# Kernel tuning notes

Measured on AMD Instinct MI355X. Metric: run time of the kernel, lower is better.

The kernel has to match this reference:

```python
import jax, jax.numpy as jnp
import numpy as np

B, NQ, C, H, W, HEADS = 8, 300, 256, 64, 64, 8
HD = C // HEADS
SCALING = float(HD) ** (-0.5)


def setup_inputs() -> dict:
    key = jax.random.key(0)
    ks = jax.random.split(key, 12)
    pts = jax.random.uniform(ks[3], (B, NQ, 2), jnp.float32)
    pts = pts * jnp.array([W - 1, H - 1], jnp.float32)  # (x, y) in pixel coords
    s = 1.0 / np.sqrt(C)
    return {
        "query": jax.random.normal(ks[0], (B, NQ, C), jnp.float32),
        "key": jax.random.normal(ks[1], (B, C, H, W), jnp.float32),
        "value": jax.random.normal(ks[2], (B, C, H, W), jnp.float32),
        "sampling_points": pts,
        "Wq": jax.random.normal(ks[4], (C, C), jnp.float32) * s,
        "bq": jnp.zeros((C,), jnp.float32),
        "Wk": jax.random.normal(ks[5], (C, C), jnp.float32) * s,
        "bk": jnp.zeros((C,), jnp.float32),
        "Wv": jax.random.normal(ks[6], (C, C), jnp.float32) * s,
        "bv": jnp.zeros((C,), jnp.float32),
        "Wo": jax.random.normal(ks[7], (C, C), jnp.float32) * s,
        "bo": jnp.zeros((C,), jnp.float32),
    }


def _sample_rows(feat, y):
    # feat: [b,heads,hd,h,w]; y: [b,q] float row coordinate.
    # Returns feat linearly interpolated in y for every column: [b,q,heads,hd,w]
    h = feat.shape[3]
    y0f = jnp.clip(jnp.floor(y), 0.0, h - 1)
    wy = y - y0f
    y0 = y0f.astype(jnp.int32)
    y1 = jnp.clip(y0 + 1, 0, h - 1)
    g = jax.vmap(lambda f, idx: f[:, :, idx, :])  # per-batch -> [heads,hd,q,w]
    r = g(feat, y0) * (1.0 - wy)[:, None, None, :, None] + g(feat, y1) * wy[:, None, None, :, None]
    return jnp.transpose(r, (0, 3, 1, 2, 4))


def _sample_cols(feat, x):
    # feat: [b,heads,hd,h,w]; x: [b,q] float col coordinate -> [b,q,heads,hd,h]
    w = feat.shape[4]
    x0f = jnp.clip(jnp.floor(x), 0.0, w - 1)
    wx = x - x0f
    x0 = x0f.astype(jnp.int32)
    x1 = jnp.clip(x0 + 1, 0, w - 1)
    g = jax.vmap(lambda f, idx: f[:, :, :, idx])  # per-batch -> [heads,hd,h,q]
    c = g(feat, x0) * (1.0 - wx)[:, None, None, None, :] + g(feat, x1) * wx[:, None, None, None, :]
    return jnp.transpose(c, (0, 4, 1, 2, 3))


def reference(query, key, value, sampling_points, Wq, bq, Wk, bk, Wv, bv, Wo, bo):
    b, nq, c = query.shape
    h, w = key.shape[2], key.shape[3]
    pq = (query @ Wq.T + bq) * SCALING                     # [b,nq,C]
    pk = jnp.einsum('oc,bchw->bohw', Wk, key) + bk[None, :, None, None]
    pv = jnp.einsum('oc,bchw->bohw', Wv, value) + bv[None, :, None, None]
    pq = pq.reshape(b, nq, HEADS, HD)
    pk = pk.reshape(b, HEADS, HD, h, w)
    pv = pv.reshape(b, HEADS, HD, h, w)
    x, y = sampling_points[..., 0], sampling_points[..., 1]
    # criss-cross weights: row through y (w samples) + column through x (h samples)
    k_row = _sample_rows(pk, y)                            # [b,q,heads,hd,w]
    k_col = _sample_cols(pk, x)                            # [b,q,heads,hd,h]
    w_row = jnp.einsum('bqnd,bqndw->bqnw', pq, k_row)
    w_col = jnp.einsum('bqnd,bqndk->bqnk', pq, k_col)
    attn = jax.nn.softmax(jnp.concatenate([w_row, w_col], axis=-1), axis=-1)
    a_row, a_col = attn[..., :w], attn[..., w:]
    v_row = _sample_rows(pv, y)
    v_col = _sample_cols(pv, x)
    out = jnp.einsum('bqnw,bqndw->bqnd', a_row, v_row) + jnp.einsum('bqnk,bqndk->bqnd', a_col, v_col)
    out = out.reshape(b, nq, c)
    return out @ Wo.T + bo
```

## Files before the change

kernel.cpp:

```cpp
#include <hip/hip_runtime.h>
#include <hip/hip_bf16.h>
#include <math.h>

constexpr int cB = 8, cNQ = 300, cC = 256, cH = 64, cW = 64, cHEADS = 8, cHD = 32;
constexpr int cHW = cH * cW;
constexpr int cM = cB * cNQ;
constexpr float cSCALE = 0.1767766952966369f;

typedef __bf16 bf16_t;
typedef bf16_t bf16x4 __attribute__((ext_vector_type(4)));
typedef bf16_t bf16x8 __attribute__((ext_vector_type(8)));
typedef float f32x4 __attribute__((ext_vector_type(4)));
typedef _Float16 f16_t;
typedef f16_t f16x2 __attribute__((ext_vector_type(2)));
typedef f16_t f16x8 __attribute__((ext_vector_type(8)));

__device__ __forceinline__ float dot2acc(f16x2 a, f16x2 b, float c) {
#if __has_builtin(__builtin_amdgcn_fdot2)
  return __builtin_amdgcn_fdot2(a, b, c, false);
#else
  return c + (float)a.x * (float)b.x + (float)a.y * (float)b.y;
#endif
}

__global__ __launch_bounds__(256) void proj_mfma_k(
    const float* __restrict__ X, const float* __restrict__ Wt,
    const float* __restrict__ bias, float* __restrict__ out,
    f16_t* __restrict__ out_h, float scale, int M) {
  __shared__ bf16_t Xs[128 * 64];
  __shared__ bf16_t Ws[64 * 64];
  int m0 = blockIdx.x * 128;
  int o0 = blockIdx.y * 64;
  int tid = threadIdx.x;
  int lane = tid & 63, w = tid >> 6;
  int moff = (w & 1) * 64, ooff = (w >> 1) * 32;
  int l15 = lane & 15, l4 = lane >> 4;
  int srow = tid >> 1;
  int schalf = (tid & 1) * 32;
  int wo_l = tid >> 2;
  int wcg = (tid & 3) * 16;

  f32x4 acc[4][2];
#pragma unroll
  for (int m = 0; m < 4; ++m)
#pragma unroll
    for (int n = 0; n < 2; ++n) acc[m][n] = (f32x4){0.f, 0.f, 0.f, 0.f};

  for (int c0 = 0; c0 < cC; c0 += 64) {
    {
      int mrow = min(m0 + srow, M - 1);
      const float4* xr = (const float4*)(X + (size_t)mrow * cC + c0 + schalf);
      int sw = (srow & 7) * 8;
#pragma unroll
      for (int i = 0; i < 4; ++i) {
        float4 a = xr[i * 2], b4 = xr[i * 2 + 1];
        bf16x8 v = {(bf16_t)a.x, (bf16_t)a.y, (bf16_t)a.z, (bf16_t)a.w,
                    (bf16_t)b4.x, (bf16_t)b4.y, (bf16_t)b4.z, (bf16_t)b4.w};
        *(bf16x8*)&Xs[srow * 64 + ((schalf + i * 8) ^ sw)] = v;
      }
    }
    {
      const float4* wr = (const float4*)(Wt + (size_t)(o0 + wo_l) * cC + c0 + wcg);
      float4 a = wr[0], b4 = wr[1], c4 = wr[2], d4 = wr[3];
      bf16x8 w0 = {(bf16_t)a.x, (bf16_t)a.y, (bf16_t)a.z, (bf16_t)a.w,
                   (bf16_t)b4.x, (bf16_t)b4.y, (bf16_t)b4.z, (bf16_t)b4.w};
      bf16x8 w1 = {(bf16_t)c4.x, (bf16_t)c4.y, (bf16_t)c4.z, (bf16_t)c4.w,
                   (bf16_t)d4.x, (bf16_t)d4.y, (bf16_t)d4.z, (bf16_t)d4.w};
      int sw = (wo_l & 7) * 8;
      *(bf16x8*)&Ws[wo_l * 64 + (wcg ^ sw)] = w0;
      *(bf16x8*)&Ws[wo_l * 64 + ((wcg + 8) ^ sw)] = w1;
    }
    __syncthreads();
#pragma unroll
    for (int s = 0; s < 2; ++s) {
      int c8 = s * 32 + l4 * 8;
      bf16x8 afr[4], bfr[2];
#pragma unroll
      for (int m = 0; m < 4; ++m) {
        int r = moff + m * 16 + l15;
        afr[m] = *(const bf16x8*)&Xs[r * 64 + (c8 ^ ((r & 7) * 8))];
      }
#pragma unroll
      for (int n = 0; n < 2; ++n) {
        int r = ooff + n * 16 + l15;
        bfr[n] = *(const bf16x8*)&Ws[r * 64 + (c8 ^ ((r & 7) * 8))];
      }
#pragma unroll
      for (int m = 0; m < 4; ++m)
#pragma unroll
        for (int n = 0; n < 2; ++n)
          acc[m][n] = __builtin_amdgcn_mfma_f32_16x16x32_bf16(
              afr[m], bfr[n], acc[m][n], 0, 0, 0);
    }
    __syncthreads();
  }

  float b0 = bias[o0 + ooff + l15];
  float b1 = bias[o0 + ooff + 16 + l15];
#pragma unroll
  for (int m = 0; m < 4; ++m) {
    int mr = m0 + moff + m * 16 + l4 * 4;
#pragma unroll
    for (int reg = 0; reg < 4; ++reg) {
      if (mr + reg < M) {
        float v0 = (acc[m][0][reg] + b0) * scale;
        float v1 = (acc[m][1][reg] + b1) * scale;
        if (out_h) {
          out_h[(size_t)(mr + reg) * cC + o0 + ooff + l15] = (f16_t)v0;
          out_h[(size_t)(mr + reg) * cC + o0 + ooff + 16 + l15] = (f16_t)v1;
        } else {
          out[(size_t)(mr + reg) * cC + o0 + ooff + l15] = v0;
          out[(size_t)(mr + reg) * cC + o0 + ooff + 16 + l15] = v1;
        }
      }
    }
  }
}

__global__ __launch_bounds__(512) void proj_kv_mfma_k(
    const float* __restrict__ key, const float* __restrict__ value,
    const float* __restrict__ Wk, const float* __restrict__ bk,
    const float* __restrict__ Wv, const float* __restrict__ bv,
    f16_t* __restrict__ pkT, f16_t* __restrict__ pvT) {
  int z = blockIdx.z;
  int b = z >> 1;
  bool isv = z & 1;
  const float* X = (isv ? value : key) + (size_t)b * cC * cHW;
  const float* Wm = isv ? Wv : Wk;
  const float* bb = isv ? bv : bk;
  f16_t* outT = (isv ? pvT : pkT) + (size_t)b * cHEADS * cHW * cHD;
  int hw0 = blockIdx.x * 128;
  int o0 = blockIdx.y * 128;

  __shared__ bf16_t Xs[2][128 * 64];
  __shared__ bf16_t Wf[2][16 * 64 * 8];

  int tid = threadIdx.x;
  int lane = tid & 63, w = tid >> 6;
  int l15 = lane & 15, l4 = lane >> 4;
  int cq = tid & 15;
  int hwg = tid >> 4;
  int wo_l = tid >> 2;
  int wcg = (tid & 3) * 16;
  int wks = wcg >> 5;
  int wl4 = (wcg & 31) >> 3;
  int wnt = wo_l >> 4, wl15 = wo_l & 15;
  int hwoff = (w >> 2) * 64;
  int nb = (w & 3) * 2;

  const float* xbase = X + hw0 + hwg * 4;
  const float* wbase = Wm + (size_t)(o0 + wo_l) * cC + wcg;

  f32x4 acc[4][2];
#pragma unroll
  for (int m = 0; m < 4; ++m)
#pragma unroll
    for (int n = 0; n < 2; ++n) acc[m][n] = (f32x4){0.f, 0.f, 0.f, 0.f};

  float4 xr4[4];
  float4 wr[4];
  auto issue = [&](int c0) {
#pragma unroll
    for (int i = 0; i < 4; ++i)
      xr4[i] = *(const float4*)(xbase + (size_t)(c0 + cq * 4 + i) * cHW);
    const float4* p = (const float4*)(wbase + c0);
    wr[0] = p[0]; wr[1] = p[1]; wr[2] = p[2]; wr[3] = p[3];
  };

  issue(0);
#pragma unroll
  for (int s = 0; s < 4; ++s) {
    const int buf = s & 1;
#pragma unroll
    for (int j = 0; j < 4; ++j) {
      int row = hwg * 4 + j;
      bf16x4 v = {(bf16_t)xr4[0][j], (bf16_t)xr4[1][j],
                  (bf16_t)xr4[2][j], (bf16_t)xr4[3][j]};
      *(bf16x4*)&Xs[buf][row * 64 + ((cq * 4) ^ ((row & 7) * 8))] = v;
    }
    {
      bf16x8 v0 = {(bf16_t)wr[0].x, (bf16_t)wr[0].y, (bf16_t)wr[0].z, (bf16_t)wr[0].w,
                   (bf16_t)wr[1].x, (bf16_t)wr[1].y, (bf16_t)wr[1].z, (bf16_t)wr[1].w};
      bf16x8 v1 = {(bf16_t)wr[2].x, (bf16_t)wr[2].y, (bf16_t)wr[2].z, (bf16_t)wr[2].w,
                   (bf16_t)wr[3].x, (bf16_t)wr[3].y, (bf16_t)wr[3].z, (bf16_t)wr[3].w};
      *(bf16x8*)&Wf[buf][(size_t)((wks * 8 + wnt) * 64 + wl4 * 16 + wl15) * 8] = v0;
      *(bf16x8*)&Wf[buf][(size_t)((wks * 8 + wnt) * 64 + (wl4 + 1) * 16 + wl15) * 8] = v1;
    }
    if (s < 3) issue((s + 1) * 64);
    __syncthreads();
#pragma unroll
    for (int ks = 0; ks < 2; ++ks) {
      int c8 = ks * 32 + l4 * 8;
      bf16x8 bf0 = *(const bf16x8*)&Wf[buf][(size_t)((ks * 8 + nb) * 64 + lane) * 8];
      bf16x8 bf1 = *(const bf16x8*)&Wf[buf][(size_t)((ks * 8 + nb + 1) * 64 + lane) * 8];
#pragma unroll
      for (int m = 0; m < 4; ++m) {
        int r = hwoff + m * 16 + l15;
        bf16x8 a = *(const bf16x8*)&Xs[buf][r * 64 + (c8 ^ ((r & 7) * 8))];
        acc[m][0] = __builtin_amdgcn_mfma_f32_16x16x32_bf16(a, bf0, acc[m][0], 0, 0, 0);
        acc[m][1] = __builtin_amdgcn_mfma_f32_16x16x32_bf16(a, bf1, acc[m][1], 0, 0, 0);
      }
    }
  }

  int osub = o0 + nb * 16;
  int head = osub >> 5;
  f16_t* obase = outT + (size_t)head * cHW * cHD;
  float bias0 = bb[osub + l15];
  float bias1 = bb[osub + 16 + l15];
#pragma unroll
  for (int m = 0; m < 4; ++m) {
    int hwr = hwoff + m * 16 + l4 * 4;
#pragma unroll
    for (int reg = 0; reg < 4; ++reg) {
      int hw = hw0 + hwr + reg;
      size_t rowoff = (size_t)hw * cHD;
      obase[rowoff + l15] = (f16_t)(acc[m][0][reg] + bias0);
      obase[rowoff + 16 + l15] = (f16_t)(acc[m][1][reg] + bias1);
    }
  }
}

__global__ __launch_bounds__(256) void attn_k(
    const f16_t* __restrict__ pqh, const f16_t* __restrict__ pkT,
    const f16_t* __restrict__ pvT, const float* __restrict__ pts,
    float* __restrict__ out) {
  int bid = blockIdx.x;
  int xcd = bid & 7;
  int t = bid >> 3;
  int phase = (t >= cNQ) ? 1 : 0;
  int q = t - phase * cNQ;
  int g = xcd + 8 * phase;
  int b = g >> 1;
  int pair = g & 1;
  int lane = threadIdx.x & 63;
  int wid = threadIdx.x >> 6;
  int n = pair * 4 + wid;

  float x = pts[((size_t)b * cNQ + q) * 2 + 0];
  float y = pts[((size_t)b * cNQ + q) * 2 + 1];
  float y0f = fminf(fmaxf(floorf(y), 0.f), (float)(cH - 1));
  float x0f = fminf(fmaxf(floorf(x), 0.f), (float)(cW - 1));
  float wy = y - y0f, wx = x - x0f;
  int y0 = (int)y0f, y1 = min(y0 + 1, cH - 1);
  int x0 = (int)x0f, x1 = min(x0 + 1, cW - 1);

  size_t hoff = (size_t)(b * cHEADS + n) * cHW * cHD;
  const f16_t* kTb = pkT + hoff;
  const f16_t* vTb = pvT + hoff;

  int g16 = lane >> 2, ch = lane & 3;

  f16x8 qv = *(const f16x8*)(pqh + ((size_t)b * cNQ + q) * cC + n * cHD + ch * 8);
  const f16x2* qp = (const f16x2*)&qv;

  float wrowA[4], wcolA[4];
#pragma unroll
  for (int k = 0; k < 4; ++k) {
    int p = g16 * 4 + k;
    f16x8 a0 = *(const f16x8*)(kTb + (size_t)(y0 * cW + p) * cHD + ch * 8);
    f16x8 a1 = *(const f16x8*)(kTb + (size_t)(y1 * cW + p) * cHD + ch * 8);
    f16x8 b0 = *(const f16x8*)(kTb + (size_t)(p * cW + x0) * cHD + ch * 8);
    f16x8 b1 = *(const f16x8*)(kTb + (size_t)(p * cW + x1) * cHD + ch * 8);
    const f16x2* a0p = (const f16x2*)&a0;
    const f16x2* a1p = (const f16x2*)&a1;
    const f16x2* b0p = (const f16x2*)&b0;
    const f16x2* b1p = (const f16x2*)&b1;
    float s0 = 0.f, s1 = 0.f, t0 = 0.f, t1 = 0.f;
#pragma unroll
    for (int j2 = 0; j2 < 4; ++j2) {
      f16x2 qq = qp[j2];
      s0 = dot2acc(a0p[j2], qq, s0);
      s1 = dot2acc(a1p[j2], qq, s1);
      t0 = dot2acc(b0p[j2], qq, t0);
      t1 = dot2acc(b1p[j2], qq, t1);
    }
    float wrow = s0 + wy * (s1 - s0);
    float wcol = t0 + wx * (t1 - t0);
    wrow += __shfl_xor(wrow, 1, 64);
    wrow += __shfl_xor(wrow, 2, 64);
    wcol += __shfl_xor(wcol, 1, 64);
    wcol += __shfl_xor(wcol, 2, 64);
    wrowA[k] = wrow;
    wcolA[k] = wcol;
  }

  float m = -1e30f;
#pragma unroll
  for (int k = 0; k < 4; ++k) m = fmaxf(m, fmaxf(wrowA[k], wcolA[k]));
#pragma unroll
  for (int sh = 4; sh <= 32; sh <<= 1) m = fmaxf(m, __shfl_xor(m, sh, 64));
  float er[4], ec[4];
  float ssl = 0.f;
#pragma unroll
  for (int k = 0; k < 4; ++k) {
    er[k] = __expf(wrowA[k] - m);
    ec[k] = __expf(wcolA[k] - m);
    ssl += er[k] + ec[k];
  }
  float ssum = ssl;
#pragma unroll
  for (int sh = 4; sh <= 32; sh <<= 1) ssum += __shfl_xor(ssum, sh, 64);

  float omwy = 1.f - wy, omwx = 1.f - wx;
  float acc[8];
#pragma unroll
  for (int j = 0; j < 8; ++j) acc[j] = 0.f;
#pragma unroll
  for (int k = 0; k < 4; ++k) {
    int p = g16 * 4 + k;
    f16x8 r0 = *(const f16x8*)(vTb + (size_t)(y0 * cW + p) * cHD + ch * 8);
    f16x8 r1 = *(const f16x8*)(vTb + (size_t)(y1 * cW + p) * cHD + ch * 8);
    f16x8 c0 = *(const f16x8*)(vTb + (size_t)(p * cW + x0) * cHD + ch * 8);
    f16x8 c1 = *(const f16x8*)(vTb + (size_t)(p * cW + x1) * cHD + ch * 8);
    float wr0 = er[k] * omwy, wr1 = er[k] * wy;
    float wc0 = ec[k] * omwx, wc1 = ec[k] * wx;
#pragma unroll
    for (int j = 0; j < 8; ++j) {
      acc[j] += wr0 * (float)r0[j] + wr1 * (float)r1[j] +
                wc0 * (float)c0[j] + wc1 * (float)c1[j];
    }
  }
#pragma unroll
  for (int sh = 4; sh <= 32; sh <<= 1)
#pragma unroll
    for (int j = 0; j < 8; ++j) acc[j] += __shfl_xor(acc[j], sh, 64);

  float inv = 1.f / ssum;
  if (lane < 4) {
    float* op = out + ((size_t)b * cNQ + q) * cC + n * cHD + ch * 8;
    float4 o0 = {acc[0] * inv, acc[1] * inv, acc[2] * inv, acc[3] * inv};
    float4 o1 = {acc[4] * inv, acc[5] * inv, acc[6] * inv, acc[7] * inv};
    *(float4*)op = o0;
    *(float4*)(op + 4) = o1;
  }
}

extern "C" void kernel_launch(void* const* d_in, const int* in_sizes, int n_in,
                              void* d_out, int out_size, void* d_ws, size_t ws_size,
                              hipStream_t stream) {
  const float* query = (const float*)d_in[0];
  const float* key   = (const float*)d_in[1];
  const float* value = (const float*)d_in[2];
  const float* pts   = (const float*)d_in[3];
  const float* Wq = (const float*)d_in[4];
  const float* bq = (const float*)d_in[5];
  const float* Wk = (const float*)d_in[6];
  const float* bk = (const float*)d_in[7];
  const float* Wv = (const float*)d_in[8];
  const float* bv = (const float*)d_in[9];
  const float* Wo = (const float*)d_in[10];
  const float* bo = (const float*)d_in[11];
  float* out = (float*)d_out;

  const size_t kvsz = (size_t)cB * cC * cHW;
  f16_t* pqh = (f16_t*)d_ws;
  f16_t* pkT = pqh + (size_t)cM * cC;
  f16_t* pvT = pkT + kvsz;
  float* ao = (float*)(pvT + kvsz);

  proj_mfma_k<<<dim3((cM + 127) / 128, cC / 64), 256, 0, stream>>>(
      query, Wq, bq, nullptr, pqh, cSCALE, cM);
  proj_kv_mfma_k<<<dim3(cHW / 128, cC / 128, cB * 2), 512, 0, stream>>>(
      key, value, Wk, bk, Wv, bv, pkT, pvT);
  attn_k<<<cB * cNQ * 2, 256, 0, stream>>>(pqh, pkT, pvT, pts, ao);
  proj_mfma_k<<<dim3((cM + 127) / 128, cC / 64), 256, 0, stream>>>(
      ao, Wo, bo, out, nullptr, 1.0f, cM);
}
```

Measured before the change: 92.68 us.

## Overlap second-half K/V projection with first-half attention in a merged kernel

Splits the K/V projection by batch. The first four batches are projected alone. A merged kernel then interleaves blocks that project the last four batches with blocks that run attention for the first four batches, and a final kernel does attention for the remaining batches. The aim is to overlap compute-heavy MFMA projection with the gather-heavy attention and to cut idle time between dependent launches. In exchange it adds an extra synchronisation per projection stage, and the merged blocks reserve the full 512-thread and shared-memory footprint even on attention blocks, which may reduce occupancy.

```diff
diff --git a/kernel.cpp b/kernel.cpp
--- a/kernel.cpp
+++ b/kernel.cpp
@@ -117,25 +117,22 @@
   }
 }
 
-__global__ __launch_bounds__(512) void proj_kv_mfma_k(
+__device__ __forceinline__ void proj_kv_body(
+    int xb, int yb, int zb, int tid,
     const float* __restrict__ key, const float* __restrict__ value,
     const float* __restrict__ Wk, const float* __restrict__ bk,
     const float* __restrict__ Wv, const float* __restrict__ bv,
-    f16_t* __restrict__ pkT, f16_t* __restrict__ pvT) {
-  int z = blockIdx.z;
-  int b = z >> 1;
-  bool isv = z & 1;
+    f16_t* __restrict__ pkT, f16_t* __restrict__ pvT,
+    bf16_t* __restrict__ XsB, bf16_t* __restrict__ WfB) {
+  int b = zb >> 1;
+  bool isv = zb & 1;
   const float* X = (isv ? value : key) + (size_t)b * cC * cHW;
   const float* Wm = isv ? Wv : Wk;
   const float* bb = isv ? bv : bk;
   f16_t* outT = (isv ? pvT : pkT) + (size_t)b * cHEADS * cHW * cHD;
-  int hw0 = blockIdx.x * 128;
-  int o0 = blockIdx.y * 128;
-
-  __shared__ bf16_t Xs[2][128 * 64];
-  __shared__ bf16_t Wf[2][16 * 64 * 8];
-
-  int tid = threadIdx.x;
+  int hw0 = xb * 128;
+  int o0 = yb * 128;
+
   int lane = tid & 63, w = tid >> 6;
   int l15 = lane & 15, l4 = lane >> 4;
   int cq = tid & 15;
@@ -170,37 +167,39 @@
   issue(0);
 #pragma unroll
   for (int s = 0; s < 4; ++s) {
-    const int buf = s & 1;
+    bf16_t* Xs = XsB + (s & 1) * (128 * 64);
+    bf16_t* Wf = WfB + (s & 1) * (16 * 64 * 8);
 #pragma unroll
     for (int j = 0; j < 4; ++j) {
       int row = hwg * 4 + j;
       bf16x4 v = {(bf16_t)xr4[0][j], (bf16_t)xr4[1][j],
                   (bf16_t)xr4[2][j], (bf16_t)xr4[3][j]};
-      *(bf16x4*)&Xs[buf][row * 64 + ((cq * 4) ^ ((row & 7) * 8))] = v;
+      *(bf16x4*)&Xs[row * 64 + ((cq * 4) ^ ((row & 7) * 8))] = v;
     }
     {
       bf16x8 v0 = {(bf16_t)wr[0].x, (bf16_t)wr[0].y, (bf16_t)wr[0].z, (bf16_t)wr[0].w,
                    (bf16_t)wr[1].x, (bf16_t)wr[1].y, (bf16_t)wr[1].z, (bf16_t)wr[1].w};
       bf16x8 v1 = {(bf16_t)wr[2].x, (bf16_t)wr[2].y, (bf16_t)wr[2].z, (bf16_t)wr[2].w,
                    (bf16_t)wr[3].x, (bf16_t)wr[3].y, (bf16_t)wr[3].z, (bf16_t)wr[3].w};
-      *(bf16x8*)&Wf[buf][(size_t)((wks * 8 + wnt) * 64 + wl4 * 16 + wl15) * 8] = v0;
-      *(bf16x8*)&Wf[buf][(size_t)((wks * 8 + wnt) * 64 + (wl4 + 1) * 16 + wl15) * 8] = v1;
+      *(bf16x8*)&Wf[(size_t)((wks * 8 + wnt) * 64 + wl4 * 16 + wl15) * 8] = v0;
+      *(bf16x8*)&Wf[(size_t)((wks * 8 + wnt) * 64 + (wl4 + 1) * 16 + wl15) * 8] = v1;
     }
     if (s < 3) issue((s + 1) * 64);
     __syncthreads();
 #pragma unroll
     for (int ks = 0; ks < 2; ++ks) {
       int c8 = ks * 32 + l4 * 8;
-      bf16x8 bf0 = *(const bf16x8*)&Wf[buf][(size_t)((ks * 8 + nb) * 64 + lane) * 8];
-      bf16x8 bf1 = *(const bf16x8*)&Wf[buf][(size_t)((ks * 8 + nb + 1) * 64 + lane) * 8];
+      bf16x8 bf0 = *(const bf16x8*)&Wf[(size_t)((ks * 8 + nb) * 64 + lane) * 8];
+      bf16x8 bf1 = *(const bf16x8*)&Wf[(size_t)((ks * 8 + nb + 1) * 64 + lane) * 8];
 #pragma unroll
       for (int m = 0; m < 4; ++m) {
         int r = hwoff + m * 16 + l15;
-        bf16x8 a = *(const bf16x8*)&Xs[buf][r * 64 + (c8 ^ ((r & 7) * 8))];
+        bf16x8 a = *(const bf16x8*)&Xs[r * 64 + (c8 ^ ((r & 7) * 8))];
         acc[m][0] = __builtin_amdgcn_mfma_f32_16x16x32_bf16(a, bf0, acc[m][0], 0, 0, 0);
         acc[m][1] = __builtin_amdgcn_mfma_f32_16x16x32_bf16(a, bf1, acc[m][1], 0, 0, 0);
       }
     }
+    if (s < 3) __syncthreads();
   }
 
   int osub = o0 + nb * 16;
@@ -221,20 +220,13 @@
   }
 }
 
-__global__ __launch_bounds__(256) void attn_k(
+__device__ __forceinline__ void attn_body(
+    int b, int pair, int q, int subtid,
     const f16_t* __restrict__ pqh, const f16_t* __restrict__ pkT,
     const f16_t* __restrict__ pvT, const float* __restrict__ pts,
     float* __restrict__ out) {
-  int bid = blockIdx.x;
-  int xcd = bid & 7;
-  int t = bid >> 3;
-  int phase = (t >= cNQ) ? 1 : 0;
-  int q = t - phase * cNQ;
-  int g = xcd + 8 * phase;
-  int b = g >> 1;
-  int pair = g & 1;
-  int lane = threadIdx.x & 63;
-  int wid = threadIdx.x >> 6;
+  int lane = subtid & 63;
+  int wid = subtid >> 6;
   int n = pair * 4 + wid;
 
   float x = pts[((size_t)b * cNQ + q) * 2 + 0];
@@ -334,6 +326,55 @@
     *(float4*)op = o0;
     *(float4*)(op + 4) = o1;
   }
+}
+
+__global__ __launch_bounds__(512) void proj_kv_half_k(
+    const float* __restrict__ key, const float* __restrict__ value,
+    const float* __restrict__ Wk, const float* __restrict__ bk,
+    const float* __restrict__ Wv, const float* __restrict__ bv,
+    f16_t* __restrict__ pkT, f16_t* __restrict__ pvT, int zbase) {
+  __shared__ bf16_t Xs[2][128 * 64];
+  __shared__ bf16_t Wf[2][16 * 64 * 8];
+  proj_kv_body(blockIdx.x, blockIdx.y, zbase + blockIdx.z, threadIdx.x,
+               key, value, Wk, bk, Wv, bv, pkT, pvT, &Xs[0][0], &Wf[0][0]);
+}
+
+__global__ __launch_bounds__(512) void merged_k(
+    const float* __restrict__ key, const float* __restrict__ value,
+    const float* __restrict__ Wk, const float* __restrict__ bk,
+    const float* __restrict__ Wv, const float* __restrict__ bv,
+    f16_t* __restrict__ pkT, f16_t* __restrict__ pvT,
+    const f16_t* __restrict__ pqh, const float* __restrict__ pts,
+    float* __restrict__ ao) {
+  __shared__ bf16_t Xs[2][128 * 64];
+  __shared__ bf16_t Wf[2][16 * 64 * 8];
+  int bid = blockIdx.x;
+  int g = bid >> 3, sub8 = bid & 7;
+  int npg = (g * 32) / 107;
+  bool is_proj = ((g + 1) * 32) / 107 > npg;
+  if (is_proj) {
+    int p = npg * 8 + sub8;
+    proj_kv_body(p & 31, (p >> 5) & 1, 8 + (p >> 6), threadIdx.x,
+                 key, value, Wk, bk, Wv, bv, pkT, pvT, &Xs[0][0], &Wf[0][0]);
+  } else {
+    int ag = g - npg;
+    int b = sub8 >> 1;
+    int pair = sub8 & 1;
+    int q = ag * 2 + (threadIdx.x >> 8);
+    attn_body(b, pair, q, threadIdx.x & 255, pqh, pkT, pvT, pts, ao);
+  }
+}
+
+__global__ __launch_bounds__(256) void attn_half_k(
+    const f16_t* __restrict__ pqh, const f16_t* __restrict__ pkT,
+    const f16_t* __restrict__ pvT, const float* __restrict__ pts,
+    float* __restrict__ out, int b_off) {
+  int bid = blockIdx.x;
+  int gxcd = bid & 7;
+  int b = b_off + (gxcd >> 1);
+  int pair = gxcd & 1;
+  int q = bid >> 3;
+  attn_body(b, pair, q, threadIdx.x, pqh, pkT, pvT, pts, out);
 }
 
 extern "C" void kernel_launch(void* const* d_in, const int* in_sizes, int n_in,
@@ -361,9 +402,11 @@
 
   proj_mfma_k<<<dim3((cM + 127) / 128, cC / 64), 256, 0, stream>>>(
       query, Wq, bq, nullptr, pqh, cSCALE, cM);
-  proj_kv_mfma_k<<<dim3(cHW / 128, cC / 128, cB * 2), 512, 0, stream>>>(
-      key, value, Wk, bk, Wv, bv, pkT, pvT);
-  attn_k<<<cB * cNQ * 2, 256, 0, stream>>>(pqh, pkT, pvT, pts, ao);
+  proj_kv_half_k<<<dim3(32, 2, 8), 512, 0, stream>>>(
+      key, value, Wk, bk, Wv, bv, pkT, pvT, 0);
+  merged_k<<<214 * 8, 512, 0, stream>>>(
+      key, value, Wk, bk, Wv, bv, pkT, pvT, pqh, pts, ao);
+  attn_half_k<<<2400, 256, 0, stream>>>(pqh, pkT, pvT, pts, ao, 4);
   proj_mfma_k<<<dim3((cM + 127) / 128, cC / 64), 256, 0, stream>>>(
       ao, Wo, bo, out, nullptr, 1.0f, cM);
 }
```

Result: slower. 101.9 us (+10.0%).
